# Kernel tuning notes

Hardware: AMD Instinct MI355X
Metric: run time of the kernel (lower is better)

Reference implementation:

```python
import jax, jax.numpy as jnp
import numpy as np

E = 384          # embed_dim
NH = 12          # num_heads
HD = E // NH     # head_dim = 32
NC = 16          # num_clusters
SCALE = HD ** -0.5


def setup_inputs() -> dict:
    key = jax.random.key(0)
    ks = jax.random.split(key, 6)
    b, h, w = 8, 64, 64
    x = jax.random.normal(ks[0], (b, E, h, w), jnp.float32)
    qkv_w = jax.random.normal(ks[1], (3 * E, E), jnp.float32) * 0.02
    qkv_b = jnp.zeros((3 * E,), jnp.float32)
    lepe_w = jax.random.normal(ks[2], (E, 1, 5, 5), jnp.float32) * 0.02
    lepe_b = jnp.zeros((E,), jnp.float32)
    out_w = jax.random.normal(ks[3], (E, E), jnp.float32) * 0.02
    out_b = jnp.zeros((E,), jnp.float32)
    return dict(x=x, qkv_w=qkv_w, qkv_b=qkv_b, lepe_w=lepe_w,
                lepe_b=lepe_b, out_w=out_w, out_b=out_b)


def _gather_tokens(t, idx):
    # t: (b, n, l, d), idx: (b, n, l)
    return jnp.take_along_axis(t, idx[..., None], axis=2)


def reference(x, qkv_w, qkv_b, lepe_w, lepe_b, out_w, out_b):
    b, _, h, w = x.shape
    l = h * w
    lc = l // NC  # tokens per cluster

    # 1x1 conv qkv projection (channel order: [q heads | k heads | v heads])
    qkv = jnp.einsum('bchw,oc->bohw', x, qkv_w) + qkv_b[None, :, None, None]

    # lepe: 5x5 depthwise conv on the v channel slice
    v_img = qkv[:, 2 * E:]
    lepe = jax.lax.conv_general_dilated(
        v_img, lepe_w, (1, 1), ((2, 2), (2, 2)),
        feature_group_count=E,
        dimension_numbers=('NCHW', 'OIHW', 'NCHW')) + lepe_b[None, :, None, None]

    # 'b (m n d) h w -> m b n (h w) d'
    qkv = qkv.reshape(b, 3, NH, HD, l).transpose(1, 0, 2, 4, 3)  # (3,b,n,l,d)
    q, k, v = qkv[0], qkv[1], qkv[2]
    k = k * SCALE

    # cosine-similarity sort routing (sort_sim(k, k))
    cls = jnp.mean(k, axis=2, keepdims=True)                       # (b,n,1,d)
    cls = cls / jnp.maximum(jnp.linalg.norm(cls, axis=-1, keepdims=True), 1e-12)
    kn = k / jnp.maximum(jnp.linalg.norm(k, axis=-1, keepdims=True), 1e-12)
    cos = jnp.einsum('bnod,bnld->bnl', cls, kn)                    # (b,n,l)
    idx = jnp.argsort(cos, axis=-1)                                # (b,n,l)

    qs = _gather_tokens(q, idx).reshape(b, NH, NC, lc, HD)
    ks_ = _gather_tokens(k, idx).reshape(b, NH, NC, lc, HD)
    vs = _gather_tokens(v, idx).reshape(b, NH, NC, lc, HD)

    # blockwise (per-cluster) attention
    attn = jax.nn.softmax(jnp.einsum('bncld,bncmd->bnclm', qs, ks_), axis=-1)
    o = jnp.einsum('bnclm,bncmd->bncld', attn, vs).reshape(b, NH, l, HD)

    # restore original token order (inverse permutation)
    inv = jnp.argsort(idx, axis=-1)
    o = _gather_tokens(o, inv)

    # 'b n (h w) d -> b (n d) h w'
    o = o.transpose(0, 1, 3, 2).reshape(b, E, h, w)

    res = o + lepe
    return jnp.einsum('bchw,oc->bohw', res, out_w) + out_b[None, :, None, None]
```

## Files before the change

### kernel.cpp

```cpp
#include <hip/hip_runtime.h>
#include <math.h>

#define SCALE_F   0.17677669529663687f
#define SCALE_L2E 0.25505837072959003f

using bf16x8 = __attribute__((ext_vector_type(8))) __bf16;
using f32x2  = __attribute__((ext_vector_type(2))) float;
using f32x4  = __attribute__((ext_vector_type(4))) float;
using f32x16 = __attribute__((ext_vector_type(16))) float;
using uint2e = __attribute__((ext_vector_type(2))) unsigned int;

__device__ inline unsigned short f2bf(float x) {
    __bf16 h = (__bf16)x;
    return __builtin_bit_cast(unsigned short, h);
}
__device__ inline float bf2f(unsigned short u) {
    unsigned int x = ((unsigned int)u) << 16;
    return __builtin_bit_cast(float, x);
}
__device__ inline unsigned int packbf(float a, float b) {
    return (unsigned int)f2bf(a) | ((unsigned int)f2bf(b) << 16);
}
__device__ inline bf16x8 ldfrag(const unsigned short* p) {
    return __builtin_bit_cast(bf16x8, *reinterpret_cast<const uint4*>(p));
}

__global__ __launch_bounds__(512)
void gemm_k_kernel(const float* __restrict__ A, const float* __restrict__ Bmat,
                   const float* __restrict__ bias, float* __restrict__ CT)
{
    const int bm = blockIdx.x, bn = blockIdx.y, bz = blockIdx.z;
    const float* Bp = Bmat + (long)bz * 384 * 4096;
    float* Cp = CT + (long)bz * 4096 * 384;
    __shared__ float As[32][132];
    __shared__ float BsF[32 * 136];
    const int tid = threadIdx.x;
    const int tx = tid & 15, ty = tid >> 4;
    const int m0 = bm * 128, n0 = bn * 128;

    f32x2 acc2[4][4];
    #pragma unroll
    for (int i = 0; i < 4; ++i)
        #pragma unroll
        for (int p = 0; p < 4; ++p) acc2[i][p] = (f32x2){0.f, 0.f};

    for (int k0 = 0; k0 < 384; k0 += 32) {
        if (k0) __syncthreads();
        #pragma unroll
        for (int it = 0; it < 2; ++it) {
            int slot = tid + it * 512;
            int rA = slot >> 3, cA = slot & 7;
            float4 av = *reinterpret_cast<const float4*>(&A[(long)(384 + m0 + rA) * 384 + k0 + cA * 4]);
            As[cA * 4 + 0][rA] = av.x; As[cA * 4 + 1][rA] = av.y;
            As[cA * 4 + 2][rA] = av.z; As[cA * 4 + 3][rA] = av.w;
            int sr = slot >> 5, sq = slot & 31;
            int wB = sr * 136 + ((sq & 1) << 6) + ((sq >> 1) << 2);
            *reinterpret_cast<float4*>(&BsF[wB]) =
                *reinterpret_cast<const float4*>(&Bp[(long)(k0 + sr) * 4096 + n0 + sq * 4]);
        }
        __syncthreads();
        #pragma unroll
        for (int kk = 0; kk < 32; ++kk) {
            float a[4];
            *reinterpret_cast<float4*>(&a[0]) = *reinterpret_cast<const float4*>(&As[kk][ty * 4]);
            float4 blo = *reinterpret_cast<const float4*>(&BsF[kk * 136 + tx * 4]);
            float4 bhi = *reinterpret_cast<const float4*>(&BsF[kk * 136 + 64 + tx * 4]);
            f32x2 b2[4];
            b2[0] = (f32x2){blo.x, blo.y}; b2[1] = (f32x2){blo.z, blo.w};
            b2[2] = (f32x2){bhi.x, bhi.y}; b2[3] = (f32x2){bhi.z, bhi.w};
            #pragma unroll
            for (int i = 0; i < 4; ++i) {
                f32x2 a2 = (f32x2){a[i], a[i]};
                #pragma unroll
                for (int p = 0; p < 4; ++p)
                    acc2[i][p] = __builtin_elementwise_fma(a2, b2[p], acc2[i][p]);
            }
        }
    }

    float bv[4];
    #pragma unroll
    for (int i = 0; i < 4; ++i) bv[i] = bias[384 + m0 + ty * 4 + i];
    #pragma unroll
    for (int p = 0; p < 4; ++p)
        #pragma unroll
        for (int c = 0; c < 2; ++c) {
            int j = 2 * p + c;
            long tok = n0 + tx * 8 + j;
            float4 v = make_float4(acc2[0][p][c] + bv[0], acc2[1][p][c] + bv[1],
                                   acc2[2][p][c] + bv[2], acc2[3][p][c] + bv[3]);
            *reinterpret_cast<float4*>(Cp + tok * 384 + m0 + ty * 4) = v;
        }
}

template<bool SPLIT, int SM>
__global__ __launch_bounds__(256)
void mfma_nt_kernel(const unsigned short* __restrict__ Ah, const unsigned short* __restrict__ Al,
                    const unsigned short* __restrict__ Bh, const unsigned short* __restrict__ Bl,
                    const float* __restrict__ bias, void* __restrict__ Cout,
                    int K, int lda, int ldb,
                    long strideAb, long strideBb, long strideCb)
{
    extern __shared__ unsigned short smem[];
    unsigned short* As  = smem;
    unsigned short* Bs  = smem + 5120;
    unsigned short* Asl = smem + 10240;
    unsigned short* Bsl = smem + 15360;
    const int bm = blockIdx.x, bn = blockIdx.y, bz = blockIdx.z;
    const unsigned short* Ap = Ah + (long)bz * strideAb;
    const unsigned short* Bp = Bh + (long)bz * strideBb;
    const unsigned short* Alp = nullptr;
    const unsigned short* Blp = nullptr;
    if constexpr (SPLIT) {
        Alp = Al + (long)bz * strideAb;
        Blp = Bl + (long)bz * strideBb;
    }
    const int tid = threadIdx.x;
    const int lane = tid & 63, wid = tid >> 6;
    const int wr = wid >> 1, wc = wid & 1;
    const int l15 = lane & 15, l4 = lane >> 4;
    const int m0 = bm * 128, n0 = bn * 128;

    const f32x4 Z4 = {0.f, 0.f, 0.f, 0.f};
    f32x4 acc[4][4];
    #pragma unroll
    for (int i = 0; i < 4; ++i)
        #pragma unroll
        for (int j = 0; j < 4; ++j) acc[i][j] = Z4;

    for (int k0 = 0; k0 < K; k0 += 32) {
        if (k0) __syncthreads();
        #pragma unroll
        for (int it = 0; it < 2; ++it) {
            int slot = tid + it * 256;
            int r = slot >> 2, cq = slot & 3;
            *reinterpret_cast<uint4*>(&As[r * 40 + cq * 8]) =
                *reinterpret_cast<const uint4*>(&Ap[(long)(m0 + r) * lda + k0 + cq * 8]);
            *reinterpret_cast<uint4*>(&Bs[r * 40 + cq * 8]) =
                *reinterpret_cast<const uint4*>(&Bp[(long)(n0 + r) * ldb + k0 + cq * 8]);
            if constexpr (SPLIT) {
                *reinterpret_cast<uint4*>(&Asl[r * 40 + cq * 8]) =
                    *reinterpret_cast<const uint4*>(&Alp[(long)(m0 + r) * lda + k0 + cq * 8]);
                *reinterpret_cast<uint4*>(&Bsl[r * 40 + cq * 8]) =
                    *reinterpret_cast<const uint4*>(&Blp[(long)(n0 + r) * ldb + k0 + cq * 8]);
            }
        }
        __syncthreads();

        bf16x8 af[4], bg[4], afl[4], bgl[4];
        #pragma unroll
        for (int f = 0; f < 4; ++f) {
            af[f] = ldfrag(&As[(wr * 64 + f * 16 + l15) * 40 + l4 * 8]);
            bg[f] = ldfrag(&Bs[(wc * 64 + f * 16 + l15) * 40 + l4 * 8]);
        }
        if constexpr (SPLIT) {
            #pragma unroll
            for (int f = 0; f < 4; ++f) {
                afl[f] = ldfrag(&Asl[(wr * 64 + f * 16 + l15) * 40 + l4 * 8]);
                bgl[f] = ldfrag(&Bsl[(wc * 64 + f * 16 + l15) * 40 + l4 * 8]);
            }
        }
        #pragma unroll
        for (int fi = 0; fi < 4; ++fi)
            #pragma unroll
            for (int fj = 0; fj < 4; ++fj) {
                acc[fi][fj] = __builtin_amdgcn_mfma_f32_16x16x32_bf16(af[fi], bg[fj], acc[fi][fj], 0, 0, 0);
                if constexpr (SPLIT) {
                    acc[fi][fj] = __builtin_amdgcn_mfma_f32_16x16x32_bf16(af[fi], bgl[fj], acc[fi][fj], 0, 0, 0);
                    acc[fi][fj] = __builtin_amdgcn_mfma_f32_16x16x32_bf16(afl[fi], bg[fj], acc[fi][fj], 0, 0, 0);
                }
            }
    }

    if constexpr (SM == 0) {
        unsigned short* Cq = (unsigned short*)Cout + (long)bz * strideCb;
        #pragma unroll
        for (int fi = 0; fi < 4; ++fi)
            #pragma unroll
            for (int fj = 0; fj < 4; ++fj) {
                const int m = m0 + wr * 64 + fi * 16 + l4 * 4;
                const int t = n0 + wc * 64 + fj * 16 + l15;
                ushort4 h;
                h.x = f2bf(acc[fi][fj][0] + bias[m + 0]);
                h.y = f2bf(acc[fi][fj][1] + bias[m + 1]);
                h.z = f2bf(acc[fi][fj][2] + bias[m + 2]);
                h.w = f2bf(acc[fi][fj][3] + bias[m + 3]);
                *reinterpret_cast<ushort4*>(&Cq[(long)t * 768 + m]) = h;
            }
    } else {
        float* Cf = (float*)Cout + (long)bz * strideCb;
        #pragma unroll
        for (int fi = 0; fi < 4; ++fi)
            #pragma unroll
            for (int fj = 0; fj < 4; ++fj) {
                const int t = m0 + wr * 64 + fi * 16 + l4 * 4;
                const int m = n0 + wc * 64 + fj * 16 + l15;
                const float bv = bias[m];
                float4 v = make_float4(acc[fi][fj][0] + bv, acc[fi][fj][1] + bv,
                                       acc[fi][fj][2] + bv, acc[fi][fj][3] + bv);
                *reinterpret_cast<float4*>(&Cf[(long)m * 4096 + t]) = v;
            }
    }
}

__global__ __launch_bounds__(256)
void convert_w_kernel(const float* __restrict__ qkv_w, const float* __restrict__ qkv_b,
                      const float* __restrict__ out_w,
                      unsigned short* __restrict__ Wqv, float* __restrict__ qvb,
                      unsigned short* __restrict__ owh, unsigned short* __restrict__ owl)
{
    const int total = 294912 + 147456 + 768;
    for (int i = blockIdx.x * 256 + threadIdx.x; i < total; i += gridDim.x * 256) {
        if (i < 294912) {
            int m = i / 384, k = i - m * 384;
            int src = (m < 384) ? m : m + 384;
            Wqv[i] = f2bf(qkv_w[(long)src * 384 + k]);
        } else if (i < 294912 + 147456) {
            int o = i - 294912;
            float w = out_w[o];
            unsigned short h = f2bf(w);
            owh[o] = h;
            owl[o] = f2bf(w - bf2f(h));
        } else {
            int m = i - 294912 - 147456;
            qvb[m] = qkv_b[(m < 384) ? m : m + 384];
        }
    }
}

__global__ __launch_bounds__(256)
void transpose_x_kernel(const float* __restrict__ x, unsigned short* __restrict__ xbT)
{
    const int t0 = blockIdx.x * 64, c0 = blockIdx.y * 64, b = blockIdx.z;
    __shared__ float tl[64][65];
    const int tid = threadIdx.x;
    #pragma unroll
    for (int i = 0; i < 16; ++i) {
        int cr = (tid >> 6) + i * 4, tc = tid & 63;
        tl[cr][tc] = x[((long)b * 384 + c0 + cr) * 4096 + t0 + tc];
    }
    __syncthreads();
    #pragma unroll
    for (int i = 0; i < 8; ++i) {
        int tr = (tid >> 5) + i * 8, c2 = (tid & 31) * 2;
        unsigned int u = packbf(tl[c2][tr], tl[c2 + 1][tr]);
        *reinterpret_cast<unsigned int*>(&xbT[((long)b * 4096 + t0 + tr) * 384 + c0 + c2]) = u;
    }
}

__global__ __launch_bounds__(256)
void lepe_kernel(const unsigned short* __restrict__ qvB, const float* __restrict__ w5,
                 const float* __restrict__ wb, unsigned short* __restrict__ lepeT)
{
    const int ch0 = blockIdx.x * 16;
    const int y0 = blockIdx.y * 8;
    const int b = blockIdx.z;
    const unsigned short* vb = qvB + (long)b * 4096 * 768 + 384 + ch0;
    unsigned short* dst = lepeT + (long)b * 4096 * 384 + ch0;
    __shared__ float tile[12 * 68 * 16];
    const int tid = threadIdx.x;

    for (int s = tid; s < 12 * 68 * 2; s += 256) {
        int pix = s >> 1, half = s & 1;
        int yy = pix / 68, xx = pix % 68;
        int gy = y0 + yy - 2, gx = xx - 2;
        float* tp = &tile[pix * 16 + half * 8];
        if (gy >= 0 && gy < 64 && gx >= 0 && gx < 64) {
            uint4 u = *reinterpret_cast<const uint4*>(vb + (long)(gy * 64 + gx) * 768 + half * 8);
            tp[0] = bf2f((unsigned short)(u.x & 0xFFFFu)); tp[1] = bf2f((unsigned short)(u.x >> 16));
            tp[2] = bf2f((unsigned short)(u.y & 0xFFFFu)); tp[3] = bf2f((unsigned short)(u.y >> 16));
            tp[4] = bf2f((unsigned short)(u.z & 0xFFFFu)); tp[5] = bf2f((unsigned short)(u.z >> 16));
            tp[6] = bf2f((unsigned short)(u.w & 0xFFFFu)); tp[7] = bf2f((unsigned short)(u.w >> 16));
        } else {
            #pragma unroll
            for (int j = 0; j < 8; ++j) tp[j] = 0.f;
        }
    }
    const int c = tid & 15, xo = tid >> 4;
    float f[25];
    #pragma unroll
    for (int j = 0; j < 25; ++j) f[j] = w5[(ch0 + c) * 25 + j];
    const float bv = wb[ch0 + c];
    __syncthreads();

    #pragma unroll
    for (int yy = 0; yy < 8; ++yy) {
        #pragma unroll
        for (int xq = 0; xq < 4; ++xq) {
            int x = xq * 16 + xo;
            float acc = bv;
            #pragma unroll
            for (int dy = 0; dy < 5; ++dy)
                #pragma unroll
                for (int dx = 0; dx < 5; ++dx)
                    acc += tile[((yy + dy) * 68 + (x + dx)) * 16 + c] * f[dy * 5 + dx];
            dst[(long)((y0 + yy) * 64 + x) * 384 + c] = f2bf(acc);
        }
    }
}

__global__ __launch_bounds__(256)
void cls_kernel(const float* __restrict__ Kf32, float* __restrict__ clsg)
{
    const int bn = blockIdx.x;
    const int b = bn / 12, n = bn % 12;
    const float* kb = Kf32 + (long)b * 4096 * 384 + n * 32;
    __shared__ float part[256][33];
    const int tid = threadIdx.x;
    float acc[32];
    #pragma unroll
    for (int d = 0; d < 32; ++d) acc[d] = 0.f;
    for (int i = 0; i < 16; ++i) {
        long tok = tid + i * 256;
        const float* kr = kb + tok * 384;
        #pragma unroll
        for (int d = 0; d < 32; ++d) acc[d] += kr[d];
    }
    #pragma unroll
    for (int d = 0; d < 32; ++d) part[tid][d] = acc[d];
    __syncthreads();
    if (tid < 32) {
        double s = 0.0;
        for (int t = 0; t < 256; ++t) s += (double)part[t][tid];
        part[0][tid] = (float)s;
    }
    __syncthreads();
    if (tid == 0) {
        double nn = 0.0;
        for (int d = 0; d < 32; ++d) { double v = (double)part[0][d]; nn += v * v; }
        double inv = 1.0 / sqrt(nn > 1e-300 ? nn : 1e-300);
        for (int d = 0; d < 32; ++d) clsg[bn * 32 + d] = (float)((double)part[0][d] * inv);
    }
}

__global__ __launch_bounds__(256)
void cos2_kernel(const float* __restrict__ Kf32, const float* __restrict__ clsg,
                 float* __restrict__ cosv)
{
    const int bn = blockIdx.x;
    const int b = bn / 12, n = bn % 12;
    const float* kb = Kf32 + (long)b * 4096 * 384 + n * 32;
    const int t0 = blockIdx.y * 512;
    const int tid = threadIdx.x;
    float clsn[32];
    #pragma unroll
    for (int d = 0; d < 32; ++d) clsn[d] = clsg[bn * 32 + d];
    #pragma unroll
    for (int i = 0; i < 2; ++i) {
        long tok = t0 + tid + i * 256;
        const float* kr = kb + tok * 384;
        double dot = 0.0, nrm = 0.0;
        #pragma unroll
        for (int d = 0; d < 32; ++d) {
            float kv = kr[d];
            dot += (double)clsn[d] * (double)kv;
            nrm += (double)kv * (double)kv;
        }
        double cv = dot / sqrt(nrm > 1e-300 ? nrm : 1e-300);
        cosv[(long)bn * 4096 + tok] = (float)cv;
    }
}

__global__ __launch_bounds__(1024)
void sort_kernel(const float* __restrict__ cosv, int* __restrict__ idxo)
{
    const int bn = blockIdx.x;
    __shared__ unsigned long long sk[4096];
    const int tid = threadIdx.x;
    for (int i = tid; i < 4096; i += 1024) {
        unsigned int u = __builtin_bit_cast(unsigned int, cosv[(long)bn * 4096 + i]);
        u = (u & 0x80000000u) ? ~u : (u | 0x80000000u);
        sk[i] = ((unsigned long long)u << 32) | (unsigned int)i;
    }
    __syncthreads();
    for (int size = 2; size <= 4096; size <<= 1) {
        for (int stride = size >> 1; stride >= 1; stride >>= 1) {
            #pragma unroll 2
            for (int i = tid; i < 2048; i += 1024) {
                int lo = (i << 1) - (i & (stride - 1));
                int hi = lo + stride;
                bool asc = ((lo & size) == 0);
                unsigned long long a = sk[lo], bq = sk[hi];
                if ((a > bq) == asc) { sk[lo] = bq; sk[hi] = a; }
            }
            __syncthreads();
        }
    }
    for (int i = tid; i < 4096; i += 1024)
        idxo[(long)bn * 4096 + i] = (int)(sk[i] & 0xFFFFFFFFu);
}

__global__ __launch_bounds__(256)
void attn_kernel(const float* __restrict__ Kf32, unsigned short* __restrict__ qvB,
                 const int* __restrict__ idxbuf, const unsigned short* __restrict__ lepeT)
{
    const int cc = blockIdx.x, n = blockIdx.y, b = blockIdx.z;
    const int* ip = idxbuf + ((long)(b * 12 + n)) * 4096 + cc * 256;

    __shared__ unsigned short KsL[256][36];
    __shared__ unsigned short VsT[32][260];
    __shared__ int tokLds[256];

    const int tid = threadIdx.x;
    const int w = tid >> 6;
    const int lane = tid & 63;
    const int lo5 = lane & 31;
    const int hi = lane >> 5;
    const int hi8 = hi * 8;

    const int tk0 = ip[tid];
    tokLds[tid] = tk0;
    const long tb = (long)b * 4096 + tk0;
    const unsigned short* qrow = qvB + tb * 768 + n * 32;
    const float* krow = Kf32 + tb * 384 + n * 32;

    unsigned int Pq[16];
    #pragma unroll
    for (int i = 0; i < 4; ++i) {
        uint4 qu = *reinterpret_cast<const uint4*>(qrow + i * 8);
        Pq[4 * i + 0] = qu.x; Pq[4 * i + 1] = qu.y;
        Pq[4 * i + 2] = qu.z; Pq[4 * i + 3] = qu.w;
    }
    #pragma unroll
    for (int dq = 0; dq < 8; ++dq) {
        float4 kv = *reinterpret_cast<const float4*>(krow + dq * 4);
        ushort4 kp;
        kp.x = f2bf(kv.x * SCALE_L2E); kp.y = f2bf(kv.y * SCALE_L2E);
        kp.z = f2bf(kv.z * SCALE_L2E); kp.w = f2bf(kv.w * SCALE_L2E);
        *reinterpret_cast<ushort4*>(&KsL[tid][dq * 4]) = kp;
    }
    {
        union { uint4 u[4]; unsigned short s[32]; } vv;
        const unsigned short* vrow = qrow + 384;
        #pragma unroll
        for (int i = 0; i < 4; ++i) vv.u[i] = *reinterpret_cast<const uint4*>(vrow + i * 8);
        #pragma unroll
        for (int j = 0; j < 32; ++j) VsT[j][tid] = vv.s[j];
    }

    bf16x8 qf00, qf01, qf10, qf11;
    {
        unsigned int w0[2][4], w1[2][4];
        #pragma unroll
        for (int ks = 0; ks < 2; ++ks)
            #pragma unroll
            for (int j = 0; j < 4; ++j) {
                uint2e r = __builtin_amdgcn_permlane32_swap(Pq[ks * 8 + j], Pq[ks * 8 + 4 + j], false, false);
                w0[ks][j] = r[0];
                w1[ks][j] = r[1];
            }
        qf00 = __builtin_bit_cast(bf16x8, make_uint4(w0[0][0], w0[0][1], w0[0][2], w0[0][3]));
        qf01 = __builtin_bit_cast(bf16x8, make_uint4(w0[1][0], w0[1][1], w0[1][2], w0[1][3]));
        qf10 = __builtin_bit_cast(bf16x8, make_uint4(w1[0][0], w1[0][1], w1[0][2], w1[0][3]));
        qf11 = __builtin_bit_cast(bf16x8, make_uint4(w1[1][0], w1[1][1], w1[1][2], w1[1][3]));
    }
    __syncthreads();

    const f32x16 Z16 = {0,0,0,0,0,0,0,0,0,0,0,0,0,0,0,0};
    f32x16 o0 = Z16, o1 = Z16;
    float lsum0 = 0.f, lsum1 = 0.f;

#define LDFRAG(ARR, ROW, OFF) ({ \
    const unsigned short* _p = &ARR[ROW][OFF]; \
    union { bf16x8 v; ushort4 h[2]; } _u; \
    _u.h[0] = *reinterpret_cast<const ushort4*>(_p); \
    _u.h[1] = *reinterpret_cast<const ushort4*>(_p + 4); \
    _u.v; })

#define EXP16(S, LS) { _Pragma("unroll") for (int r = 0; r < 16; ++r) { float _e = __builtin_exp2f(S[r]); S[r] = _e; LS += _e; } }

#define MKPB(S, H) ({ \
    unsigned int _x0 = packbf(S[(H) * 8 + 0], S[(H) * 8 + 1]); \
    unsigned int _x1 = packbf(S[(H) * 8 + 2], S[(H) * 8 + 3]); \
    unsigned int _x2 = packbf(S[(H) * 8 + 4], S[(H) * 8 + 5]); \
    unsigned int _x3 = packbf(S[(H) * 8 + 6], S[(H) * 8 + 7]); \
    uint2e _r02 = __builtin_amdgcn_permlane32_swap(_x0, _x2, false, false); \
    uint2e _r13 = __builtin_amdgcn_permlane32_swap(_x1, _x3, false, false); \
    __builtin_bit_cast(bf16x8, make_uint4(_r02[0], _r13[0], _r02[1], _r13[1])); })

    for (int ch = 0; ch < 4; ++ch) {
        const int rb = ch * 64;
        f32x16 s00 = Z16, s01 = Z16, s10 = Z16, s11 = Z16;
        bf16x8 ka;
        __builtin_amdgcn_s_setprio(1);
        ka = LDFRAG(KsL, rb + lo5, hi8);
        s00 = __builtin_amdgcn_mfma_f32_32x32x16_bf16(ka, qf00, s00, 0, 0, 0);
        s01 = __builtin_amdgcn_mfma_f32_32x32x16_bf16(ka, qf10, s01, 0, 0, 0);
        ka = LDFRAG(KsL, rb + lo5, 16 + hi8);
        s00 = __builtin_amdgcn_mfma_f32_32x32x16_bf16(ka, qf01, s00, 0, 0, 0);
        s01 = __builtin_amdgcn_mfma_f32_32x32x16_bf16(ka, qf11, s01, 0, 0, 0);
        ka = LDFRAG(KsL, rb + 32 + lo5, hi8);
        s10 = __builtin_amdgcn_mfma_f32_32x32x16_bf16(ka, qf00, s10, 0, 0, 0);
        s11 = __builtin_amdgcn_mfma_f32_32x32x16_bf16(ka, qf10, s11, 0, 0, 0);
        ka = LDFRAG(KsL, rb + 32 + lo5, 16 + hi8);
        s10 = __builtin_amdgcn_mfma_f32_32x32x16_bf16(ka, qf01, s10, 0, 0, 0);
        s11 = __builtin_amdgcn_mfma_f32_32x32x16_bf16(ka, qf11, s11, 0, 0, 0);
        __builtin_amdgcn_s_setprio(0);

        EXP16(s00, lsum0); EXP16(s01, lsum1);
        EXP16(s10, lsum0); EXP16(s11, lsum1);

        bf16x8 va, pb0, pb1;
        __builtin_amdgcn_s_setprio(1);
        va = LDFRAG(VsT, lo5, rb + 0 + hi8);
        pb0 = MKPB(s00, 0); pb1 = MKPB(s01, 0);
        o0 = __builtin_amdgcn_mfma_f32_32x32x16_bf16(va, pb0, o0, 0, 0, 0);
        o1 = __builtin_amdgcn_mfma_f32_32x32x16_bf16(va, pb1, o1, 0, 0, 0);
        va = LDFRAG(VsT, lo5, rb + 16 + hi8);
        pb0 = MKPB(s00, 1); pb1 = MKPB(s01, 1);
        o0 = __builtin_amdgcn_mfma_f32_32x32x16_bf16(va, pb0, o0, 0, 0, 0);
        o1 = __builtin_amdgcn_mfma_f32_32x32x16_bf16(va, pb1, o1, 0, 0, 0);
        va = LDFRAG(VsT, lo5, rb + 32 + hi8);
        pb0 = MKPB(s10, 0); pb1 = MKPB(s11, 0);
        o0 = __builtin_amdgcn_mfma_f32_32x32x16_bf16(va, pb0, o0, 0, 0, 0);
        o1 = __builtin_amdgcn_mfma_f32_32x32x16_bf16(va, pb1, o1, 0, 0, 0);
        va = LDFRAG(VsT, lo5, rb + 48 + hi8);
        pb0 = MKPB(s10, 1); pb1 = MKPB(s11, 1);
        o0 = __builtin_amdgcn_mfma_f32_32x32x16_bf16(va, pb0, o0, 0, 0, 0);
        o1 = __builtin_amdgcn_mfma_f32_32x32x16_bf16(va, pb1, o1, 0, 0, 0);
        __builtin_amdgcn_s_setprio(0);
    }

    const float lf0 = lsum0 + __shfl_xor(lsum0, 32);
    const float lf1 = lsum1 + __shfl_xor(lsum1, 32);
    const float li0 = 1.f / lf0, li1 = 1.f / lf1;

    #pragma unroll
    for (int qt = 0; qt < 2; ++qt) {
        const int qrix = w * 64 + qt * 32 + lo5;
        const int tk = tokLds[qrix];
        const long tb2 = (long)b * 4096 + tk;
        unsigned short* resrow = qvB + tb2 * 768;
        const unsigned short* lp = lepeT + tb2 * 384 + n * 32;
        const float li = qt ? li1 : li0;
        const f32x16& oo = qt ? o1 : o0;
        #pragma unroll
        for (int qd = 0; qd < 4; ++qd) {
            const int d0 = qd * 8 + hi * 4;
            ushort4 lv = *reinterpret_cast<const ushort4*>(lp + d0);
            float r0 = oo[qd * 4 + 0] * li + bf2f(lv.x);
            float r1 = oo[qd * 4 + 1] * li + bf2f(lv.y);
            float r2 = oo[qd * 4 + 2] * li + bf2f(lv.z);
            float r3 = oo[qd * 4 + 3] * li + bf2f(lv.w);
            unsigned short h0 = f2bf(r0), h1 = f2bf(r1), h2 = f2bf(r2), h3 = f2bf(r3);
            ushort4 hh = {h0, h1, h2, h3};
            ushort4 ll = {f2bf(r0 - bf2f(h0)), f2bf(r1 - bf2f(h1)),
                          f2bf(r2 - bf2f(h2)), f2bf(r3 - bf2f(h3))};
            *reinterpret_cast<ushort4*>(resrow + n * 32 + d0) = hh;
            *reinterpret_cast<ushort4*>(resrow + 384 + n * 32 + d0) = ll;
        }
    }
#undef LDFRAG
#undef EXP16
#undef MKPB
}

extern "C" void kernel_launch(void* const* d_in, const int* in_sizes, int n_in,
                              void* d_out, int out_size, void* d_ws, size_t ws_size,
                              hipStream_t stream)
{
    const float* x      = (const float*)d_in[0];
    const float* qkv_w  = (const float*)d_in[1];
    const float* qkv_b  = (const float*)d_in[2];
    const float* lepe_w = (const float*)d_in[3];
    const float* lepe_b = (const float*)d_in[4];
    const float* out_w  = (const float*)d_in[5];
    const float* out_b  = (const float*)d_in[6];
    float* out = (float*)d_out;

    char* ws = (char*)d_ws;
    float*          Kf32 = (float*)ws;
    unsigned short* qvB  = (unsigned short*)(ws + 50331648);
    float*          cosv = (float*)(ws + 100663296);
    int*            idx  = (int*)(ws + 102236160);
    unsigned short* Wqv  = (unsigned short*)(ws + 103809024);
    unsigned short* owh  = (unsigned short*)(ws + 104398848);
    unsigned short* owl  = (unsigned short*)(ws + 104693760);
    float*          qvb  = (float*)(ws + 104988672);
    float*          clsg = (float*)(ws + 104991744);

    unsigned short* xbT   = (unsigned short*)d_out;
    unsigned short* lepeT = (unsigned short*)d_out + 12582912;

    convert_w_kernel<<<1731, 256, 0, stream>>>(qkv_w, qkv_b, out_w, Wqv, qvb, owh, owl);
    transpose_x_kernel<<<dim3(64, 6, 8), 256, 0, stream>>>(x, xbT);
    gemm_k_kernel<<<dim3(3, 32, 8), 512, 0, stream>>>(qkv_w, x, qkv_b, Kf32);
    mfma_nt_kernel<false, 0><<<dim3(6, 32, 8), 256, 20480, stream>>>(
        Wqv, nullptr, xbT, nullptr, qvb, qvB,
        384, 384, 384, 0L, (long)4096 * 384, (long)4096 * 768);
    lepe_kernel<<<dim3(24, 8, 8), 256, 0, stream>>>(qvB, lepe_w, lepe_b, lepeT);
    cls_kernel<<<96, 256, 0, stream>>>(Kf32, clsg);
    cos2_kernel<<<dim3(96, 8), 256, 0, stream>>>(Kf32, clsg, cosv);
    sort_kernel<<<96, 1024, 0, stream>>>(cosv, idx);
    attn_kernel<<<dim3(16, 12, 8), 256, 0, stream>>>(Kf32, qvB, idx, lepeT);
    mfma_nt_kernel<true, 1><<<dim3(32, 3, 8), 256, 40960, stream>>>(
        qvB, qvB + 384, owh, owl, out_b, out,
        384, 768, 384, (long)4096 * 768, 0L, (long)384 * 4096);
}
```

Measured before the change: 401.3 us.

## Merge lepe conv and cosine kernels into one launch, prefetch B tile in K-GEMM

Merges the depthwise 5x5 lepe kernel and the cosine-similarity kernel into a single launch, with separate block ranges for each job. This removes one launch and lets the two independent workloads fill the GPU at the same time. Separately, the fp32 K-projection GEMM now register-prefetches the next B tile from global memory while computing the current one, to hide load latency. Costs are the extra registers used by the prefetch and the larger shared-memory footprint now carried by the cosine blocks.

Measured after the change: 395.6 us. About the same (-1.4%).

```diff
diff --git a/kernel.cpp b/kernel.cpp
--- a/kernel.cpp
+++ b/kernel.cpp
@@ -38,14 +38,24 @@
     const int tx = tid & 15, ty = tid >> 4;
     const int m0 = bm * 128, n0 = bn * 128;
 
+    const int sr0 = tid >> 5,          sq0 = tid & 31;
+    const int sr1 = (tid + 512) >> 5,  sq1 = (tid + 512) & 31;
+    const int wB0 = sr0 * 136 + ((sq0 & 1) << 6) + ((sq0 >> 1) << 2);
+    const int wB1 = sr1 * 136 + ((sq1 & 1) << 6) + ((sq1 >> 1) << 2);
+
     f32x2 acc2[4][4];
     #pragma unroll
     for (int i = 0; i < 4; ++i)
         #pragma unroll
         for (int p = 0; p < 4; ++p) acc2[i][p] = (f32x2){0.f, 0.f};
+
+    float4 bPf0 = *reinterpret_cast<const float4*>(&Bp[(long)sr0 * 4096 + n0 + sq0 * 4]);
+    float4 bPf1 = *reinterpret_cast<const float4*>(&Bp[(long)sr1 * 4096 + n0 + sq1 * 4]);
 
     for (int k0 = 0; k0 < 384; k0 += 32) {
         if (k0) __syncthreads();
+        *reinterpret_cast<float4*>(&BsF[wB0]) = bPf0;
+        *reinterpret_cast<float4*>(&BsF[wB1]) = bPf1;
         #pragma unroll
         for (int it = 0; it < 2; ++it) {
             int slot = tid + it * 512;
@@ -53,12 +63,12 @@
             float4 av = *reinterpret_cast<const float4*>(&A[(long)(384 + m0 + rA) * 384 + k0 + cA * 4]);
             As[cA * 4 + 0][rA] = av.x; As[cA * 4 + 1][rA] = av.y;
             As[cA * 4 + 2][rA] = av.z; As[cA * 4 + 3][rA] = av.w;
-            int sr = slot >> 5, sq = slot & 31;
-            int wB = sr * 136 + ((sq & 1) << 6) + ((sq >> 1) << 2);
-            *reinterpret_cast<float4*>(&BsF[wB]) =
-                *reinterpret_cast<const float4*>(&Bp[(long)(k0 + sr) * 4096 + n0 + sq * 4]);
         }
         __syncthreads();
+        if (k0 + 32 < 384) {
+            bPf0 = *reinterpret_cast<const float4*>(&Bp[(long)(k0 + 32 + sr0) * 4096 + n0 + sq0 * 4]);
+            bPf1 = *reinterpret_cast<const float4*>(&Bp[(long)(k0 + 32 + sr1) * 4096 + n0 + sq1 * 4]);
+        }
         #pragma unroll
         for (int kk = 0; kk < 32; ++kk) {
             float a[4];
@@ -249,57 +259,6 @@
 }
 
 __global__ __launch_bounds__(256)
-void lepe_kernel(const unsigned short* __restrict__ qvB, const float* __restrict__ w5,
-                 const float* __restrict__ wb, unsigned short* __restrict__ lepeT)
-{
-    const int ch0 = blockIdx.x * 16;
-    const int y0 = blockIdx.y * 8;
-    const int b = blockIdx.z;
-    const unsigned short* vb = qvB + (long)b * 4096 * 768 + 384 + ch0;
-    unsigned short* dst = lepeT + (long)b * 4096 * 384 + ch0;
-    __shared__ float tile[12 * 68 * 16];
-    const int tid = threadIdx.x;
-
-    for (int s = tid; s < 12 * 68 * 2; s += 256) {
-        int pix = s >> 1, half = s & 1;
-        int yy = pix / 68, xx = pix % 68;
-        int gy = y0 + yy - 2, gx = xx - 2;
-        float* tp = &tile[pix * 16 + half * 8];
-        if (gy >= 0 && gy < 64 && gx >= 0 && gx < 64) {
-            uint4 u = *reinterpret_cast<const uint4*>(vb + (long)(gy * 64 + gx) * 768 + half * 8);
-            tp[0] = bf2f((unsigned short)(u.x & 0xFFFFu)); tp[1] = bf2f((unsigned short)(u.x >> 16));
-            tp[2] = bf2f((unsigned short)(u.y & 0xFFFFu)); tp[3] = bf2f((unsigned short)(u.y >> 16));
-            tp[4] = bf2f((unsigned short)(u.z & 0xFFFFu)); tp[5] = bf2f((unsigned short)(u.z >> 16));
-            tp[6] = bf2f((unsigned short)(u.w & 0xFFFFu)); tp[7] = bf2f((unsigned short)(u.w >> 16));
-        } else {
-            #pragma unroll
-            for (int j = 0; j < 8; ++j) tp[j] = 0.f;
-        }
-    }
-    const int c = tid & 15, xo = tid >> 4;
-    float f[25];
-    #pragma unroll
-    for (int j = 0; j < 25; ++j) f[j] = w5[(ch0 + c) * 25 + j];
-    const float bv = wb[ch0 + c];
-    __syncthreads();
-
-    #pragma unroll
-    for (int yy = 0; yy < 8; ++yy) {
-        #pragma unroll
-        for (int xq = 0; xq < 4; ++xq) {
-            int x = xq * 16 + xo;
-            float acc = bv;
-            #pragma unroll
-            for (int dy = 0; dy < 5; ++dy)
-                #pragma unroll
-                for (int dx = 0; dx < 5; ++dx)
-                    acc += tile[((yy + dy) * 68 + (x + dx)) * 16 + c] * f[dy * 5 + dx];
-            dst[(long)((y0 + yy) * 64 + x) * 384 + c] = f2bf(acc);
-        }
-    }
-}
-
-__global__ __launch_bounds__(256)
 void cls_kernel(const float* __restrict__ Kf32, float* __restrict__ clsg)
 {
     const int bn = blockIdx.x;
@@ -334,30 +293,82 @@
 }
 
 __global__ __launch_bounds__(256)
-void cos2_kernel(const float* __restrict__ Kf32, const float* __restrict__ clsg,
-                 float* __restrict__ cosv)
-{
-    const int bn = blockIdx.x;
-    const int b = bn / 12, n = bn % 12;
-    const float* kb = Kf32 + (long)b * 4096 * 384 + n * 32;
-    const int t0 = blockIdx.y * 512;
+void cos_lepe_kernel(const float* __restrict__ Kf32, const float* __restrict__ clsg,
+                     float* __restrict__ cosv,
+                     const unsigned short* __restrict__ qvB, const float* __restrict__ w5,
+                     const float* __restrict__ wb, unsigned short* __restrict__ lepeT)
+{
+    __shared__ float tile[12 * 68 * 16];
+    const int bid = blockIdx.x;
     const int tid = threadIdx.x;
-    float clsn[32];
-    #pragma unroll
-    for (int d = 0; d < 32; ++d) clsn[d] = clsg[bn * 32 + d];
-    #pragma unroll
-    for (int i = 0; i < 2; ++i) {
-        long tok = t0 + tid + i * 256;
-        const float* kr = kb + tok * 384;
-        double dot = 0.0, nrm = 0.0;
-        #pragma unroll
-        for (int d = 0; d < 32; ++d) {
-            float kv = kr[d];
-            dot += (double)clsn[d] * (double)kv;
-            nrm += (double)kv * (double)kv;
-        }
-        double cv = dot / sqrt(nrm > 1e-300 ? nrm : 1e-300);
-        cosv[(long)bn * 4096 + tok] = (float)cv;
+
+    if (bid < 1536) {
+        const int ch0 = (bid % 24) * 16;
+        const int y0 = ((bid / 24) % 8) * 8;
+        const int b = bid / 192;
+        const unsigned short* vb = qvB + (long)b * 4096 * 768 + 384 + ch0;
+        unsigned short* dst = lepeT + (long)b * 4096 * 384 + ch0;
+
+        for (int s = tid; s < 12 * 68 * 2; s += 256) {
+            int pix = s >> 1, half = s & 1;
+            int yy = pix / 68, xx = pix % 68;
+            int gy = y0 + yy - 2, gx = xx - 2;
+            float* tp = &tile[pix * 16 + half * 8];
+            if (gy >= 0 && gy < 64 && gx >= 0 && gx < 64) {
+                uint4 u = *reinterpret_cast<const uint4*>(vb + (long)(gy * 64 + gx) * 768 + half * 8);
+                tp[0] = bf2f((unsigned short)(u.x & 0xFFFFu)); tp[1] = bf2f((unsigned short)(u.x >> 16));
+                tp[2] = bf2f((unsigned short)(u.y & 0xFFFFu)); tp[3] = bf2f((unsigned short)(u.y >> 16));
+                tp[4] = bf2f((unsigned short)(u.z & 0xFFFFu)); tp[5] = bf2f((unsigned short)(u.z >> 16));
+                tp[6] = bf2f((unsigned short)(u.w & 0xFFFFu)); tp[7] = bf2f((unsigned short)(u.w >> 16));
+            } else {
+                #pragma unroll
+                for (int j = 0; j < 8; ++j) tp[j] = 0.f;
+            }
+        }
+        const int c = tid & 15, xo = tid >> 4;
+        float f[25];
+        #pragma unroll
+        for (int j = 0; j < 25; ++j) f[j] = w5[(ch0 + c) * 25 + j];
+        const float bv = wb[ch0 + c];
+        __syncthreads();
+
+        #pragma unroll
+        for (int yy = 0; yy < 8; ++yy) {
+            #pragma unroll
+            for (int xq = 0; xq < 4; ++xq) {
+                int x = xq * 16 + xo;
+                float acc = bv;
+                #pragma unroll
+                for (int dy = 0; dy < 5; ++dy)
+                    #pragma unroll
+                    for (int dx = 0; dx < 5; ++dx)
+                        acc += tile[((yy + dy) * 68 + (x + dx)) * 16 + c] * f[dy * 5 + dx];
+                dst[(long)((y0 + yy) * 64 + x) * 384 + c] = f2bf(acc);
+            }
+        }
+    } else {
+        const int cb = bid - 1536;
+        const int bn = cb % 96;
+        const int b = bn / 12, n = bn % 12;
+        const float* kb = Kf32 + (long)b * 4096 * 384 + n * 32;
+        const int t0 = (cb / 96) * 512;
+        float clsn[32];
+        #pragma unroll
+        for (int d = 0; d < 32; ++d) clsn[d] = clsg[bn * 32 + d];
+        #pragma unroll
+        for (int i = 0; i < 2; ++i) {
+            long tok = t0 + tid + i * 256;
+            const float* kr = kb + tok * 384;
+            double dot = 0.0, nrm = 0.0;
+            #pragma unroll
+            for (int d = 0; d < 32; ++d) {
+                float kv = kr[d];
+                dot += (double)clsn[d] * (double)kv;
+                nrm += (double)kv * (double)kv;
+            }
+            double cv = dot / sqrt(nrm > 1e-300 ? nrm : 1e-300);
+            cosv[(long)bn * 4096 + tok] = (float)cv;
+        }
     }
 }
 
@@ -588,9 +599,8 @@
     mfma_nt_kernel<false, 0><<<dim3(6, 32, 8), 256, 20480, stream>>>(
         Wqv, nullptr, xbT, nullptr, qvb, qvB,
         384, 384, 384, 0L, (long)4096 * 384, (long)4096 * 768);
-    lepe_kernel<<<dim3(24, 8, 8), 256, 0, stream>>>(qvB, lepe_w, lepe_b, lepeT);
     cls_kernel<<<96, 256, 0, stream>>>(Kf32, clsg);
-    cos2_kernel<<<dim3(96, 8), 256, 0, stream>>>(Kf32, clsg, cosv);
+    cos_lepe_kernel<<<2304, 256, 0, stream>>>(Kf32, clsg, cosv, qvB, lepe_w, lepe_b, lepeT);
     sort_kernel<<<96, 1024, 0, stream>>>(cosv, idx);
     attn_kernel<<<dim3(16, 12, 8), 256, 0, stream>>>(Kf32, qvB, idx, lepeT);
     mfma_nt_kernel<true, 1><<<dim3(32, 3, 8), 256, 40960, stream>>>(
```
